# Kernel tuning notes

Hardware: AMD Instinct MI355X
Metric: run time of the kernel (lower is better)

Reference implementation:

```python
import jax, jax.numpy as jnp
import numpy as np
import math

HEADS = 16
ROPE_BASE = 10000.0


def _alibi_slopes(n):
    # power-of-2 branch of ALiBiBias._get_slopes (n=16 is a power of 2)
    start = 2.0 ** (-(2.0 ** (-(math.log2(n) - 3))))
    return np.array([start * (start ** i) for i in range(n)], dtype=np.float32)


def _rope_cos_sin(T, head_dim):
    # RotaryPositionalEmbedding: inv_freq over even indices, emb = cat(freqs, freqs)
    inv_freq = 1.0 / (ROPE_BASE ** (jnp.arange(0, head_dim, 2, dtype=jnp.float32) / head_dim))
    t = jnp.arange(T, dtype=jnp.float32)
    f = t[:, None] * inv_freq[None, :]            # (T, head_dim//2)
    emb = jnp.concatenate([f, f], axis=-1)        # (T, head_dim)
    # apply_rotary_pos_emb takes cos/sin of emb then strides [0::2]
    cos = jnp.cos(emb)[:, 0::2]                   # (T, head_dim//2)
    sin = jnp.sin(emb)[:, 0::2]
    return cos, sin


def _apply_rope(x, cos, sin):
    # x: (B,H,T,hd); cos/sin: (T, hd//2)
    x1 = x[..., 0::2]
    x2 = x[..., 1::2]
    r1 = x1 * cos - x2 * sin
    r2 = x2 * cos + x1 * sin
    # interleave back: out[...,0::2]=r1, out[...,1::2]=r2
    return jnp.stack([r1, r2], axis=-1).reshape(x.shape)


def setup_inputs() -> dict:
    key = jax.random.key(0)
    k1, k2, k3, k4 = jax.random.split(key, 4)
    B, T, C = 2, 2048, 1024
    x = jax.random.normal(k1, (B, T, C), dtype=jnp.float32)
    W_qkv = jax.random.normal(k2, (C, 3 * C), dtype=jnp.float32) * 0.02
    W_out = jax.random.normal(k3, (C, C), dtype=jnp.float32) * 0.02
    b_out = jax.random.normal(k4, (C,), dtype=jnp.float32) * 0.02
    return {"x": x, "W_qkv": W_qkv, "W_out": W_out, "b_out": b_out}


def reference(x, W_qkv, W_out, b_out):
    B, T, C = x.shape
    H = HEADS
    hd = C // H

    qkv = (x @ W_qkv).reshape(B, T, 3, H, hd)
    qkv = jnp.transpose(qkv, (2, 0, 3, 1, 4))     # (3, B, H, T, hd)
    q, k, v = qkv[0], qkv[1], qkv[2]

    cos, sin = _rope_cos_sin(T, hd)
    q = _apply_rope(q, cos, sin)
    k = _apply_rope(k, cos, sin)

    scores = jnp.einsum('bhqd,bhkd->bhqk', q, k) / jnp.sqrt(jnp.float32(hd))

    # ALiBi bias: -slope_h * |i - j|
    slopes = jnp.asarray(_alibi_slopes(H))        # (H,)
    pos = jnp.arange(T, dtype=jnp.float32)
    dist = jnp.abs(pos[None, :] - pos[:, None])   # (T, T)
    scores = scores - slopes[None, :, None, None] * dist[None, None, :, :]

    attn = jax.nn.softmax(scores, axis=-1)
    out = jnp.einsum('bhqk,bhkd->bhqd', attn, v)  # (B,H,T,hd)
    out = jnp.transpose(out, (0, 2, 1, 3)).reshape(B, T, C)
    out = out @ W_out + b_out
    return out, attn
```

## Files before the change

kernel.cpp:

```cpp
#include <hip/hip_runtime.h>
#include <hip/hip_bf16.h>

typedef __bf16 bf16_t;
typedef __bf16 bf16x8 __attribute__((ext_vector_type(8)));
typedef float floatx4 __attribute__((ext_vector_type(4)));

#define NB 2
#define NT 2048
#define NC 1024
#define NH 16
#define HD 64
#define BT (NB*NT)

__global__ void k_cvt_x(const float* __restrict__ x, bf16_t* __restrict__ xb, int n){
  int i = (blockIdx.x*blockDim.x + threadIdx.x)*4;
  if (i >= n) return;
  float4 v = *(const float4*)(x+i);
  bf16_t o[4] = {(bf16_t)v.x,(bf16_t)v.y,(bf16_t)v.z,(bf16_t)v.w};
  *(uint2*)(xb+i) = *(const uint2*)o;
}

__global__ void k_cvt_t(const float* __restrict__ in, bf16_t* __restrict__ out, int K, int N){
  __shared__ float tile[32][33];
  int tid = threadIdx.x;
  int kt = blockIdx.y*32, nt = blockIdx.x*32;
  int row = tid>>3, c4 = (tid&7)*4;
  float4 v = *(const float4*)(in + (size_t)(kt+row)*N + nt + c4);
  tile[row][c4+0]=v.x; tile[row][c4+1]=v.y; tile[row][c4+2]=v.z; tile[row][c4+3]=v.w;
  __syncthreads();
  bf16_t o[4];
  #pragma unroll
  for (int i=0;i<4;i++) o[i] = (bf16_t)tile[c4+i][row];
  *(uint2*)(out + (size_t)(nt+row)*K + kt + c4) = *(const uint2*)o;
}

template<bool BIAS, bool OUTBF>
__global__ __launch_bounds__(256) void k_gemm(
    const bf16_t* __restrict__ A, const bf16_t* __restrict__ Bt,
    void* __restrict__ Cv, const float* __restrict__ bias, int M, int N, int K){
  __shared__ __align__(16) bf16_t As[64][32];
  __shared__ __align__(16) bf16_t Bs[128][32];
  int tid = threadIdx.x;
  int wave = tid>>6, lane = tid&63, quad = lane>>4, l15 = lane&15;
  int m0 = blockIdx.y*64, n0 = blockIdx.x*128;
  int wm = (wave>>1)*32, wn = (wave&1)*64;
  floatx4 acc[2][4];
  #pragma unroll
  for(int i=0;i<2;i++)
    #pragma unroll
    for(int j=0;j<4;j++) acc[i][j] = (floatx4){0.f,0.f,0.f,0.f};
  int arow = tid>>2, ac8 = (tid&3)*8;
  const bf16_t* Ag  = A  + (size_t)(m0+arow)*K + ac8;
  const bf16_t* Bg0 = Bt + (size_t)(n0+arow)*K + ac8;
  const bf16_t* Bg1 = Bt + (size_t)(n0+arow+64)*K + ac8;
  for (int k0=0;k0<K;k0+=32){
    *(bf16x8*)&As[arow][ac8]    = *(const bf16x8*)(Ag  + k0);
    *(bf16x8*)&Bs[arow][ac8]    = *(const bf16x8*)(Bg0 + k0);
    *(bf16x8*)&Bs[arow+64][ac8] = *(const bf16x8*)(Bg1 + k0);
    __syncthreads();
    bf16x8 af[2], bfr[4];
    #pragma unroll
    for(int mi=0;mi<2;mi++) af[mi]  = *(const bf16x8*)&As[wm+mi*16+l15][quad*8];
    #pragma unroll
    for(int ni=0;ni<4;ni++) bfr[ni] = *(const bf16x8*)&Bs[wn+ni*16+l15][quad*8];
    #pragma unroll
    for(int mi=0;mi<2;mi++)
      #pragma unroll
      for(int ni=0;ni<4;ni++)
        acc[mi][ni] = __builtin_amdgcn_mfma_f32_16x16x32_bf16(af[mi], bfr[ni], acc[mi][ni],0,0,0);
    __syncthreads();
  }
  #pragma unroll
  for(int ni=0;ni<4;ni++){
    int col = n0 + wn + ni*16 + l15;
    float bv = 0.f; if (BIAS) bv = bias[col];
    #pragma unroll
    for(int mi=0;mi<2;mi++){
      int rowb = m0 + wm + mi*16 + quad*4;
      #pragma unroll
      for(int r=0;r<4;r++){
        float v = acc[mi][ni][r] + bv;
        if (OUTBF) ((bf16_t*)Cv)[(size_t)(rowb+r)*N + col] = (bf16_t)v;
        else       ((float*)Cv)[(size_t)(rowb+r)*N + col]  = v;
      }
    }
  }
}

__global__ void k_rope(const bf16_t* __restrict__ qkv, bf16_t* __restrict__ Qb,
                       bf16_t* __restrict__ Kb, bf16_t* __restrict__ Vb){
  int p = blockIdx.x*blockDim.x + threadIdx.x;
  int r = p / 1536;
  int c = (p - r*1536)*2;
  int s = c >> 10, rem = c & 1023;
  int h = rem >> 6, d = rem & 63, j = d >> 1;
  int b = r >> 11, t = r & 2047;
  float x1 = (float)qkv[(size_t)r*3072 + c];
  float x2 = (float)qkv[(size_t)r*3072 + c + 1];
  float o1, o2;
  if (s < 2){
    float freq = exp2f(-0.8304820237218406f * (float)(j & 15));
    float ang = (float)t * freq;
    float sn, cs;
    sincosf(ang, &sn, &cs);
    o1 = x1*cs - x2*sn;
    o2 = x2*cs + x1*sn;
  } else { o1 = x1; o2 = x2; }
  bf16_t* dst = (s==0) ? Qb : (s==1 ? Kb : Vb);
  bf16_t o[2] = {(bf16_t)o1, (bf16_t)o2};
  *(unsigned int*)(dst + (size_t)((b*NH + h)*NT + t)*HD + d) = *(const unsigned int*)o;
}

__global__ __launch_bounds__(256) void k_attn(
    const bf16_t* __restrict__ Qb, const bf16_t* __restrict__ Kb, const bf16_t* __restrict__ Vb,
    float* __restrict__ attn, bf16_t* __restrict__ Ob){
  __shared__ __align__(16) bf16_t Ks[32][72];
  __shared__ __align__(16) bf16_t Vt[64][40];
  __shared__ __align__(16) bf16_t Ps[4][16][40];
  int tid = threadIdx.x;
  int wave = tid>>6, lane = tid&63, quad = lane>>4, l15 = lane&15;
  int qt = blockIdx.x, bh = blockIdx.y;
  int h = bh & (NH-1);
  float slope = exp2f(-0.5f*(float)(h+1));
  int qbase = qt*64 + wave*16;
  const bf16_t* qrow = Qb + ((size_t)bh*NT + qbase + l15)*HD;
  bf16x8 qa0 = *(const bf16x8*)(qrow + quad*8);
  bf16x8 qa1 = *(const bf16x8*)(qrow + 32 + quad*8);
  int sr = tid>>3, sc8 = (tid&7)*8;
  const bf16_t* kbase = Kb + ((size_t)bh*NT + sr)*HD + sc8;
  const bf16_t* vbase = Vb + ((size_t)bh*NT + sr)*HD + sc8;
  const floatx4 z4 = {0.f,0.f,0.f,0.f};

  float lsum[4] = {0.f,0.f,0.f,0.f};
  for (int k0=0;k0<NT;k0+=32){
    *(bf16x8*)&Ks[sr][sc8] = *(const bf16x8*)(kbase + (size_t)k0*HD);
    __syncthreads();
    #pragma unroll
    for (int nt=0;nt<2;nt++){
      bf16x8 kb0 = *(const bf16x8*)&Ks[nt*16+l15][quad*8];
      bf16x8 kb1 = *(const bf16x8*)&Ks[nt*16+l15][32+quad*8];
      floatx4 sv = __builtin_amdgcn_mfma_f32_16x16x32_bf16(qa0, kb0, z4,0,0,0);
      sv = __builtin_amdgcn_mfma_f32_16x16x32_bf16(qa1, kb1, sv,0,0,0);
      int kpos = k0 + nt*16 + l15;
      #pragma unroll
      for (int r=0;r<4;r++){
        int qpos = qbase + quad*4 + r;
        float sc = sv[r]*0.125f - slope*fabsf((float)(qpos - kpos));
        lsum[r] += __expf(sc);
      }
    }
    __syncthreads();
  }
  #pragma unroll
  for (int r=0;r<4;r++){
    #pragma unroll
    for (int off=1;off<16;off<<=1) lsum[r] += __shfl_xor(lsum[r], off, 16);
  }
  float invl[4];
  #pragma unroll
  for (int r=0;r<4;r++) invl[r] = 1.f / lsum[r];

  floatx4 oacc[4] = {z4,z4,z4,z4};
  float* attnrow = attn + (size_t)bh*NT*NT;
  for (int k0=0;k0<NT;k0+=32){
    *(bf16x8*)&Ks[sr][sc8] = *(const bf16x8*)(kbase + (size_t)k0*HD);
    bf16x8 vl = *(const bf16x8*)(vbase + (size_t)k0*HD);
    #pragma unroll
    for (int i=0;i<8;i++) Vt[sc8+i][sr] = vl[i];
    __syncthreads();
    #pragma unroll
    for (int nt=0;nt<2;nt++){
      bf16x8 kb0 = *(const bf16x8*)&Ks[nt*16+l15][quad*8];
      bf16x8 kb1 = *(const bf16x8*)&Ks[nt*16+l15][32+quad*8];
      floatx4 sv = __builtin_amdgcn_mfma_f32_16x16x32_bf16(qa0, kb0, z4,0,0,0);
      sv = __builtin_amdgcn_mfma_f32_16x16x32_bf16(qa1, kb1, sv,0,0,0);
      int kpos = k0 + nt*16 + l15;
      #pragma unroll
      for (int r=0;r<4;r++){
        int qpos = qbase + quad*4 + r;
        float sc = sv[r]*0.125f - slope*fabsf((float)(qpos - kpos));
        float pv = __expf(sc) * invl[r];
        attnrow[(size_t)qpos*NT + kpos] = pv;
        Ps[wave][quad*4+r][nt*16+l15] = (bf16_t)pv;
      }
    }
    __syncthreads();
    bf16x8 pa = *(const bf16x8*)&Ps[wave][l15][quad*8];
    #pragma unroll
    for (int dt=0;dt<4;dt++){
      bf16x8 vb = *(const bf16x8*)&Vt[dt*16+l15][quad*8];
      oacc[dt] = __builtin_amdgcn_mfma_f32_16x16x32_bf16(pa, vb, oacc[dt],0,0,0);
    }
    __syncthreads();
  }
  int b = bh >> 4;
  #pragma unroll
  for (int dt=0;dt<4;dt++){
    #pragma unroll
    for (int r=0;r<4;r++){
      int t = qbase + quad*4 + r;
      Ob[(size_t)(b*NT + t)*NC + h*HD + dt*16 + l15] = (bf16_t)oacc[dt][r];
    }
  }
}

extern "C" void kernel_launch(void* const* d_in, const int* in_sizes, int n_in,
                              void* d_out, int out_size, void* d_ws, size_t ws_size,
                              hipStream_t stream){
  const float* x    = (const float*)d_in[0];
  const float* Wqkv = (const float*)d_in[1];
  const float* Wout = (const float*)d_in[2];
  const float* bout = (const float*)d_in[3];
  (void)in_sizes; (void)n_in; (void)out_size; (void)ws_size;

  char* ws = (char*)d_ws;
  size_t off = 0;
  auto alloc = [&](size_t elems)->bf16_t* {
    bf16_t* p = (bf16_t*)(ws + off);
    off += ((elems*sizeof(bf16_t) + 255)/256)*256;
    return p;
  };
  bf16_t* Xb   = alloc((size_t)BT*NC);
  bf16_t* Wqt  = alloc((size_t)3*NC*NC);
  bf16_t* Wot  = alloc((size_t)NC*NC);
  bf16_t* QKVb = alloc((size_t)BT*3*NC);
  bf16_t* Qb   = alloc((size_t)NB*NH*NT*HD);
  bf16_t* Kb   = alloc((size_t)NB*NH*NT*HD);
  bf16_t* Vb   = alloc((size_t)NB*NH*NT*HD);
  bf16_t* Ob   = alloc((size_t)BT*NC);

  k_cvt_x<<<(BT*NC/4)/256, 256, 0, stream>>>(x, Xb, BT*NC);
  k_cvt_t<<<dim3(3*NC/32, NC/32), 256, 0, stream>>>(Wqkv, Wqt, NC, 3*NC);
  k_cvt_t<<<dim3(NC/32,   NC/32), 256, 0, stream>>>(Wout, Wot, NC, NC);
  k_gemm<false,true><<<dim3(3*NC/128, BT/64), 256, 0, stream>>>(Xb, Wqt, (void*)QKVb, nullptr, BT, 3*NC, NC);
  k_rope<<<(BT*1536)/256, 256, 0, stream>>>(QKVb, Qb, Kb, Vb);
  float* attn = (float*)d_out + (size_t)BT*NC;
  k_attn<<<dim3(NT/64, NB*NH), 256, 0, stream>>>(Qb, Kb, Vb, attn, Ob);
  k_gemm<true,false><<<dim3(NC/128, BT/64), 256, 0, stream>>>(Ob, Wot, d_out, bout, BT, NC, NC);
}
```

Measured before the change: 817.3 us.

## Use direct global-to-LDS loads, XOR swizzles, larger tiles, and pre-transposed V

GEMM moves to 128x128 tiles with K-step 64, loaded through global_load_lds with XOR-swizzled LDS layouts to avoid bank conflicts. Attention widens key tiles to 64, reads V from a pre-transposed global buffer built by a new k_trv kernel, and uses exp2 with folded log2e constants. The attention probabilities are written with nontemporal stores, and one barrier per tile is removed since Ps is per-wave. RoPE skips the V section. These changes target load/transpose overhead and LDS conflicts, at the cost of an extra kernel launch and higher register pressure.

```diff
diff --git a/kernel.cpp b/kernel.cpp
--- a/kernel.cpp
+++ b/kernel.cpp
@@ -3,6 +3,7 @@
 
 typedef __bf16 bf16_t;
 typedef __bf16 bf16x8 __attribute__((ext_vector_type(8)));
+typedef __bf16 bf16x4 __attribute__((ext_vector_type(4)));
 typedef float floatx4 __attribute__((ext_vector_type(4)));
 
 #define NB 2
@@ -12,6 +13,10 @@
 #define HD 64
 #define BT (NB*NT)
 
+#define GLL16(g, l) __builtin_amdgcn_global_load_lds( \
+    (const __attribute__((address_space(1))) void*)(g), \
+    (__attribute__((address_space(3))) void*)(l), 16, 0, 0)
+
 __global__ void k_cvt_x(const float* __restrict__ x, bf16_t* __restrict__ xb, int n){
   int i = (blockIdx.x*blockDim.x + threadIdx.x)*4;
   if (i >= n) return;
@@ -34,51 +39,75 @@
   *(uint2*)(out + (size_t)(nt+row)*K + kt + c4) = *(const uint2*)o;
 }
 
+__global__ void k_trv(const bf16_t* __restrict__ qkv, bf16_t* __restrict__ Vt){
+  __shared__ float tile[32][33];
+  int tid = threadIdx.x;
+  int bh = blockIdx.z; int b = bh>>4, h = bh&15;
+  int t0 = blockIdx.y*32, d0 = blockIdx.x*32;
+  int row = tid>>3, c4 = (tid&7)*4;
+  bf16x4 v = *(const bf16x4*)(qkv + (size_t)(b*NT + t0 + row)*3072 + 2048 + h*HD + d0 + c4);
+  #pragma unroll
+  for (int i=0;i<4;i++) tile[row][c4+i] = (float)v[i];
+  __syncthreads();
+  bf16x4 o;
+  #pragma unroll
+  for (int i=0;i<4;i++) o[i] = (bf16_t)tile[c4+i][row];
+  *(bf16x4*)(Vt + ((size_t)bh*HD + d0 + row)*NT + t0 + c4) = o;
+}
+
 template<bool BIAS, bool OUTBF>
 __global__ __launch_bounds__(256) void k_gemm(
     const bf16_t* __restrict__ A, const bf16_t* __restrict__ Bt,
     void* __restrict__ Cv, const float* __restrict__ bias, int M, int N, int K){
-  __shared__ __align__(16) bf16_t As[64][32];
-  __shared__ __align__(16) bf16_t Bs[128][32];
+  __shared__ __align__(16) bf16_t As[128][64];
+  __shared__ __align__(16) bf16_t Bs[128][64];
   int tid = threadIdx.x;
   int wave = tid>>6, lane = tid&63, quad = lane>>4, l15 = lane&15;
-  int m0 = blockIdx.y*64, n0 = blockIdx.x*128;
-  int wm = (wave>>1)*32, wn = (wave&1)*64;
-  floatx4 acc[2][4];
-  #pragma unroll
-  for(int i=0;i<2;i++)
+  int m0 = blockIdx.y*128, n0 = blockIdx.x*128;
+  int wm = (wave>>1)*64, wn = (wave&1)*64;
+  floatx4 acc[4][4];
+  #pragma unroll
+  for(int i=0;i<4;i++)
     #pragma unroll
     for(int j=0;j<4;j++) acc[i][j] = (floatx4){0.f,0.f,0.f,0.f};
-  int arow = tid>>2, ac8 = (tid&3)*8;
-  const bf16_t* Ag  = A  + (size_t)(m0+arow)*K + ac8;
-  const bf16_t* Bg0 = Bt + (size_t)(n0+arow)*K + ac8;
-  const bf16_t* Bg1 = Bt + (size_t)(n0+arow+64)*K + ac8;
-  for (int k0=0;k0<K;k0+=32){
-    *(bf16x8*)&As[arow][ac8]    = *(const bf16x8*)(Ag  + k0);
-    *(bf16x8*)&Bs[arow][ac8]    = *(const bf16x8*)(Bg0 + k0);
-    *(bf16x8*)&Bs[arow+64][ac8] = *(const bf16x8*)(Bg1 + k0);
-    __syncthreads();
-    bf16x8 af[2], bfr[4];
-    #pragma unroll
-    for(int mi=0;mi<2;mi++) af[mi]  = *(const bf16x8*)&As[wm+mi*16+l15][quad*8];
-    #pragma unroll
-    for(int ni=0;ni<4;ni++) bfr[ni] = *(const bf16x8*)&Bs[wn+ni*16+l15][quad*8];
-    #pragma unroll
-    for(int mi=0;mi<2;mi++)
-      #pragma unroll
-      for(int ni=0;ni<4;ni++)
-        acc[mi][ni] = __builtin_amdgcn_mfma_f32_16x16x32_bf16(af[mi], bfr[ni], acc[mi][ni],0,0,0);
-    __syncthreads();
-  }
-  #pragma unroll
-  for(int ni=0;ni<4;ni++){
+  int srow = lane>>3;
+  int sslot = (lane&7) ^ srow;
+  const bf16_t* Ag = A  + (size_t)(m0 + wave*32 + srow)*K + sslot*8;
+  const bf16_t* Bg = Bt + (size_t)(n0 + wave*32 + srow)*K + sslot*8;
+  int rs = l15 & 7;
+  for (int k0=0; k0<K; k0+=64){
+    #pragma unroll
+    for (int i=0;i<4;i++){
+      GLL16(Ag + (size_t)(i*8)*K + k0, &As[wave*32 + i*8][0]);
+      GLL16(Bg + (size_t)(i*8)*K + k0, &Bs[wave*32 + i*8][0]);
+    }
+    __syncthreads();
+    bf16x8 af[2][4], bfr[2][4];
+    #pragma unroll
+    for (int kk=0;kk<2;kk++){
+      #pragma unroll
+      for (int mi=0;mi<4;mi++) af[kk][mi]  = *(const bf16x8*)&As[wm+mi*16+l15][8*((kk*4+quad) ^ rs)];
+      #pragma unroll
+      for (int ni=0;ni<4;ni++) bfr[kk][ni] = *(const bf16x8*)&Bs[wn+ni*16+l15][8*((kk*4+quad) ^ rs)];
+    }
+    #pragma unroll
+    for (int kk=0;kk<2;kk++)
+      #pragma unroll
+      for (int mi=0;mi<4;mi++)
+        #pragma unroll
+        for (int ni=0;ni<4;ni++)
+          acc[mi][ni] = __builtin_amdgcn_mfma_f32_16x16x32_bf16(af[kk][mi], bfr[kk][ni], acc[mi][ni],0,0,0);
+    __syncthreads();
+  }
+  #pragma unroll
+  for (int ni=0;ni<4;ni++){
     int col = n0 + wn + ni*16 + l15;
     float bv = 0.f; if (BIAS) bv = bias[col];
     #pragma unroll
-    for(int mi=0;mi<2;mi++){
+    for (int mi=0;mi<4;mi++){
       int rowb = m0 + wm + mi*16 + quad*4;
       #pragma unroll
-      for(int r=0;r<4;r++){
+      for (int r=0;r<4;r++){
         float v = acc[mi][ni][r] + bv;
         if (OUTBF) ((bf16_t*)Cv)[(size_t)(rowb+r)*N + col] = (bf16_t)v;
         else       ((float*)Cv)[(size_t)(rowb+r)*N + col]  = v;
@@ -88,108 +117,113 @@
 }
 
 __global__ void k_rope(const bf16_t* __restrict__ qkv, bf16_t* __restrict__ Qb,
-                       bf16_t* __restrict__ Kb, bf16_t* __restrict__ Vb){
+                       bf16_t* __restrict__ Kb){
   int p = blockIdx.x*blockDim.x + threadIdx.x;
-  int r = p / 1536;
-  int c = (p - r*1536)*2;
+  int r = p >> 10;
+  int c = (p & 1023)*2;
   int s = c >> 10, rem = c & 1023;
   int h = rem >> 6, d = rem & 63, j = d >> 1;
   int b = r >> 11, t = r & 2047;
   float x1 = (float)qkv[(size_t)r*3072 + c];
   float x2 = (float)qkv[(size_t)r*3072 + c + 1];
-  float o1, o2;
-  if (s < 2){
-    float freq = exp2f(-0.8304820237218406f * (float)(j & 15));
-    float ang = (float)t * freq;
-    float sn, cs;
-    sincosf(ang, &sn, &cs);
-    o1 = x1*cs - x2*sn;
-    o2 = x2*cs + x1*sn;
-  } else { o1 = x1; o2 = x2; }
-  bf16_t* dst = (s==0) ? Qb : (s==1 ? Kb : Vb);
+  float freq = exp2f(-0.8304820237218406f * (float)(j & 15));
+  float ang = (float)t * freq;
+  float sn, cs;
+  sincosf(ang, &sn, &cs);
+  float o1 = x1*cs - x2*sn;
+  float o2 = x2*cs + x1*sn;
+  bf16_t* dst = (s==0) ? Qb : Kb;
   bf16_t o[2] = {(bf16_t)o1, (bf16_t)o2};
   *(unsigned int*)(dst + (size_t)((b*NH + h)*NT + t)*HD + d) = *(const unsigned int*)o;
 }
 
 __global__ __launch_bounds__(256) void k_attn(
-    const bf16_t* __restrict__ Qb, const bf16_t* __restrict__ Kb, const bf16_t* __restrict__ Vb,
+    const bf16_t* __restrict__ Qb, const bf16_t* __restrict__ Kb, const bf16_t* __restrict__ Vtg,
     float* __restrict__ attn, bf16_t* __restrict__ Ob){
-  __shared__ __align__(16) bf16_t Ks[32][72];
-  __shared__ __align__(16) bf16_t Vt[64][40];
-  __shared__ __align__(16) bf16_t Ps[4][16][40];
+  __shared__ __align__(16) bf16_t Ks[64][64];
+  __shared__ __align__(16) bf16_t Vs[64][64];
+  __shared__ __align__(16) bf16_t Ps[4][16][64];
   int tid = threadIdx.x;
   int wave = tid>>6, lane = tid&63, quad = lane>>4, l15 = lane&15;
   int qt = blockIdx.x, bh = blockIdx.y;
   int h = bh & (NH-1);
-  float slope = exp2f(-0.5f*(float)(h+1));
+  const float LOG2E = 1.4426950408889634f;
+  float slope2 = exp2f(-0.5f*(float)(h+1)) * LOG2E;
+  const float c1 = 0.125f * LOG2E;
   int qbase = qt*64 + wave*16;
   const bf16_t* qrow = Qb + ((size_t)bh*NT + qbase + l15)*HD;
   bf16x8 qa0 = *(const bf16x8*)(qrow + quad*8);
   bf16x8 qa1 = *(const bf16x8*)(qrow + 32 + quad*8);
-  int sr = tid>>3, sc8 = (tid&7)*8;
-  const bf16_t* kbase = Kb + ((size_t)bh*NT + sr)*HD + sc8;
-  const bf16_t* vbase = Vb + ((size_t)bh*NT + sr)*HD + sc8;
+  int srow = lane>>3, sslot = (lane&7) ^ srow;
+  const bf16_t* kg = Kb  + ((size_t)bh*NT + wave*16 + srow)*HD + sslot*8;
+  const bf16_t* vg = Vtg + ((size_t)bh*HD + wave*16 + srow)*NT + sslot*8;
   const floatx4 z4 = {0.f,0.f,0.f,0.f};
+  int rs = l15 & 7;
 
   float lsum[4] = {0.f,0.f,0.f,0.f};
-  for (int k0=0;k0<NT;k0+=32){
-    *(bf16x8*)&Ks[sr][sc8] = *(const bf16x8*)(kbase + (size_t)k0*HD);
-    __syncthreads();
-    #pragma unroll
-    for (int nt=0;nt<2;nt++){
-      bf16x8 kb0 = *(const bf16x8*)&Ks[nt*16+l15][quad*8];
-      bf16x8 kb1 = *(const bf16x8*)&Ks[nt*16+l15][32+quad*8];
+  for (int k0=0;k0<NT;k0+=64){
+    #pragma unroll
+    for (int i=0;i<2;i++)
+      GLL16(kg + (size_t)(i*8)*HD + (size_t)k0*HD, &Ks[wave*16 + i*8][0]);
+    __syncthreads();
+    #pragma unroll
+    for (int nt=0;nt<4;nt++){
+      bf16x8 kb0 = *(const bf16x8*)&Ks[nt*16+l15][8*((quad)   ^ rs)];
+      bf16x8 kb1 = *(const bf16x8*)&Ks[nt*16+l15][8*((4+quad) ^ rs)];
+      floatx4 sv = __builtin_amdgcn_mfma_f32_16x16x32_bf16(qa0, kb0, z4,0,0,0);
+      sv = __builtin_amdgcn_mfma_f32_16x16x32_bf16(qa1, kb1, sv,0,0,0);
+      float fk = (float)(qbase + quad*4 - (k0 + nt*16 + l15));
+      #pragma unroll
+      for (int r=0;r<4;r++){
+        float arg = fmaf(sv[r], c1, -slope2*fabsf(fk + (float)r));
+        lsum[r] += exp2f(arg);
+      }
+    }
+    __syncthreads();
+  }
+  #pragma unroll
+  for (int r=0;r<4;r++){
+    #pragma unroll
+    for (int off=1;off<16;off<<=1) lsum[r] += __shfl_xor(lsum[r], off, 16);
+  }
+  float invl[4];
+  #pragma unroll
+  for (int r=0;r<4;r++) invl[r] = 1.f / lsum[r];
+
+  floatx4 oacc[4] = {z4,z4,z4,z4};
+  float* attnrow = attn + (size_t)bh*NT*NT;
+  for (int k0=0;k0<NT;k0+=64){
+    #pragma unroll
+    for (int i=0;i<2;i++){
+      GLL16(kg + (size_t)(i*8)*HD + (size_t)k0*HD, &Ks[wave*16 + i*8][0]);
+      GLL16(vg + (size_t)(i*8)*NT + k0,            &Vs[wave*16 + i*8][0]);
+    }
+    __syncthreads();
+    #pragma unroll
+    for (int nt=0;nt<4;nt++){
+      bf16x8 kb0 = *(const bf16x8*)&Ks[nt*16+l15][8*((quad)   ^ rs)];
+      bf16x8 kb1 = *(const bf16x8*)&Ks[nt*16+l15][8*((4+quad) ^ rs)];
       floatx4 sv = __builtin_amdgcn_mfma_f32_16x16x32_bf16(qa0, kb0, z4,0,0,0);
       sv = __builtin_amdgcn_mfma_f32_16x16x32_bf16(qa1, kb1, sv,0,0,0);
       int kpos = k0 + nt*16 + l15;
+      float fk = (float)(qbase + quad*4 - kpos);
       #pragma unroll
       for (int r=0;r<4;r++){
+        float arg = fmaf(sv[r], c1, -slope2*fabsf(fk + (float)r));
+        float pv = exp2f(arg) * invl[r];
         int qpos = qbase + quad*4 + r;
-        float sc = sv[r]*0.125f - slope*fabsf((float)(qpos - kpos));
-        lsum[r] += __expf(sc);
-      }
-    }
-    __syncthreads();
-  }
-  #pragma unroll
-  for (int r=0;r<4;r++){
-    #pragma unroll
-    for (int off=1;off<16;off<<=1) lsum[r] += __shfl_xor(lsum[r], off, 16);
-  }
-  float invl[4];
-  #pragma unroll
-  for (int r=0;r<4;r++) invl[r] = 1.f / lsum[r];
-
-  floatx4 oacc[4] = {z4,z4,z4,z4};
-  float* attnrow = attn + (size_t)bh*NT*NT;
-  for (int k0=0;k0<NT;k0+=32){
-    *(bf16x8*)&Ks[sr][sc8] = *(const bf16x8*)(kbase + (size_t)k0*HD);
-    bf16x8 vl = *(const bf16x8*)(vbase + (size_t)k0*HD);
-    #pragma unroll
-    for (int i=0;i<8;i++) Vt[sc8+i][sr] = vl[i];
-    __syncthreads();
-    #pragma unroll
-    for (int nt=0;nt<2;nt++){
-      bf16x8 kb0 = *(const bf16x8*)&Ks[nt*16+l15][quad*8];
-      bf16x8 kb1 = *(const bf16x8*)&Ks[nt*16+l15][32+quad*8];
-      floatx4 sv = __builtin_amdgcn_mfma_f32_16x16x32_bf16(qa0, kb0, z4,0,0,0);
-      sv = __builtin_amdgcn_mfma_f32_16x16x32_bf16(qa1, kb1, sv,0,0,0);
-      int kpos = k0 + nt*16 + l15;
-      #pragma unroll
-      for (int r=0;r<4;r++){
-        int qpos = qbase + quad*4 + r;
-        float sc = sv[r]*0.125f - slope*fabsf((float)(qpos - kpos));
-        float pv = __expf(sc) * invl[r];
-        attnrow[(size_t)qpos*NT + kpos] = pv;
-        Ps[wave][quad*4+r][nt*16+l15] = (bf16_t)pv;
-      }
-    }
-    __syncthreads();
-    bf16x8 pa = *(const bf16x8*)&Ps[wave][l15][quad*8];
-    #pragma unroll
-    for (int dt=0;dt<4;dt++){
-      bf16x8 vb = *(const bf16x8*)&Vt[dt*16+l15][quad*8];
-      oacc[dt] = __builtin_amdgcn_mfma_f32_16x16x32_bf16(pa, vb, oacc[dt],0,0,0);
+        __builtin_nontemporal_store(pv, &attnrow[(size_t)qpos*NT + kpos]);
+        Ps[wave][quad*4+r][ 8*(((nt*2) + (l15>>3)) ^ ((quad*4+r)&7)) + (l15&7) ] = (bf16_t)pv;
+      }
+    }
+    #pragma unroll
+    for (int ks=0;ks<2;ks++){
+      bf16x8 pa = *(const bf16x8*)&Ps[wave][l15][8*((ks*4+quad) ^ rs)];
+      #pragma unroll
+      for (int dt=0;dt<4;dt++){
+        bf16x8 vb = *(const bf16x8*)&Vs[dt*16+l15][8*((ks*4+quad) ^ rs)];
+        oacc[dt] = __builtin_amdgcn_mfma_f32_16x16x32_bf16(pa, vb, oacc[dt],0,0,0);
+      }
     }
     __syncthreads();
   }
@@ -226,15 +260,16 @@
   bf16_t* QKVb = alloc((size_t)BT*3*NC);
   bf16_t* Qb   = alloc((size_t)NB*NH*NT*HD);
   bf16_t* Kb   = alloc((size_t)NB*NH*NT*HD);
-  bf16_t* Vb   = alloc((size_t)NB*NH*NT*HD);
+  bf16_t* Vtg  = alloc((size_t)NB*NH*HD*NT);
   bf16_t* Ob   = alloc((size_t)BT*NC);
 
   k_cvt_x<<<(BT*NC/4)/256, 256, 0, stream>>>(x, Xb, BT*NC);
   k_cvt_t<<<dim3(3*NC/32, NC/32), 256, 0, stream>>>(Wqkv, Wqt, NC, 3*NC);
   k_cvt_t<<<dim3(NC/32,   NC/32), 256, 0, stream>>>(Wout, Wot, NC, NC);
-  k_gemm<false,true><<<dim3(3*NC/128, BT/64), 256, 0, stream>>>(Xb, Wqt, (void*)QKVb, nullptr, BT, 3*NC, NC);
-  k_rope<<<(BT*1536)/256, 256, 0, stream>>>(QKVb, Qb, Kb, Vb);
+  k_gemm<false,true><<<dim3(3*NC/128, BT/128), 256, 0, stream>>>(Xb, Wqt, (void*)QKVb, nullptr, BT, 3*NC, NC);
+  k_rope<<<(BT*1024)/256, 256, 0, stream>>>(QKVb, Qb, Kb);
+  k_trv<<<dim3(HD/32, NT/32, NB*NH), 256, 0, stream>>>(QKVb, Vtg);
   float* attn = (float*)d_out + (size_t)BT*NC;
-  k_attn<<<dim3(NT/64, NB*NH), 256, 0, stream>>>(Qb, Kb, Vb, attn, Ob);
-  k_gemm<true,false><<<dim3(NC/128, BT/64), 256, 0, stream>>>(Ob, Wot, d_out, bout, BT, NC, NC);
-}
+  k_attn<<<dim3(NT/64, NB*NH), 256, 0, stream>>>(Qb, Kb, Vtg, attn, Ob);
+  k_gemm<true,false><<<dim3(NC/128, BT/128), 256, 0, stream>>>(Ob, Wot, d_out, bout, BT, NC, NC);
+}
```

Result: faster. 750.1 us (-8.2%).
